# Kernel tuning notes

Hardware: AMD Instinct MI355X
Metric: run time of the kernel (lower is better)

The kernel has to match this reference:

```python
import jax, jax.numpy as jnp
import numpy as np

BATCH, SEQ, DIM = 4, 4096, 256
DT_RANK, D_STATE, NUM_TOKENS = 16, 16, 1024


def _adapool(x, T):
    # uniform window mean == AdaptiveAvgPool1d when S % T == 0
    B, S, D = x.shape
    return x.reshape(B, T, S // T, D).mean(axis=2)


def _layernorm(x, g, b, eps=1e-5):
    mu = x.mean(-1, keepdims=True)
    var = ((x - mu) ** 2).mean(-1, keepdims=True)
    return (x - mu) * jax.lax.rsqrt(var + eps) * g + b


def _gauss_mask(T):
    c = (T + 1) // 2
    idx = jnp.arange(T, dtype=jnp.float32)
    sigma = jnp.abs(idx - c).mean()
    w = jnp.exp(-0.5 * (idx - c) ** 2 / sigma ** 2)
    return w / w.sum()


def _ssm(x, Wdbc, Wdt, bdt, Alog, D):
    A = -jnp.exp(Alog)                                     # (Dm, N)
    dbc = x @ Wdbc.T                                       # (B,L,dt+2N)
    delta = jax.nn.softplus(dbc[..., :DT_RANK] @ Wdt.T + bdt)   # (B,L,Dm)
    Bm = dbc[..., DT_RANK:DT_RANK + D_STATE]               # (B,L,N)
    Cm = dbc[..., DT_RANK + D_STATE:]                      # (B,L,N)
    deltaA = jnp.exp(delta[..., None] * A)                 # (B,L,Dm,N)
    BX = (delta[..., None] * Bm[:, :, None, :]) * x[..., None]
    def comb(c1, c2):
        a1, x1 = c1
        a2, x2 = c2
        return (a2 * a1, a2 * x1 + x2)
    _, hs = jax.lax.associative_scan(comb, (deltaA, BX), axis=1)
    y = jnp.einsum('bldn,bln->bld', hs, Cm) + D * x
    return y


def setup_inputs():
    key = jax.random.key(0)
    ks = jax.random.split(key, 16)
    s = 0.05
    Alog = jnp.tile(jnp.log(jnp.arange(1.0, D_STATE + 1.0, dtype=jnp.float32))[None, :], (DIM, 1))
    return {
        'x': jax.random.normal(ks[0], (BATCH, SEQ, DIM), jnp.float32),
        'ln_g': jnp.ones((DIM,), jnp.float32),
        'ln_b': jnp.zeros((DIM,), jnp.float32),
        'W1': jax.random.normal(ks[1], (DIM, DIM), jnp.float32) * s,
        'b1': jnp.zeros((DIM,), jnp.float32),
        'W2': jax.random.normal(ks[2], (DIM, DIM), jnp.float32) * s,
        'b2': jnp.zeros((DIM,), jnp.float32),
        'Wcf': jax.random.normal(ks[3], (DIM, DIM), jnp.float32) * s,
        'bcf': jnp.zeros((DIM,), jnp.float32),
        'Wcb': jax.random.normal(ks[4], (DIM, DIM), jnp.float32) * s,
        'bcb': jnp.zeros((DIM,), jnp.float32),
        'Wdbc_f': jax.random.normal(ks[5], (DT_RANK + 2 * D_STATE, DIM), jnp.float32) * s,
        'Wdt_f': jax.random.normal(ks[6], (DIM, DT_RANK), jnp.float32) * s,
        'bdt_f': jnp.zeros((DIM,), jnp.float32),
        'Alog_f': Alog,
        'D_f': jnp.ones((DIM,), jnp.float32),
        'Wdbc_b': jax.random.normal(ks[7], (DT_RANK + 2 * D_STATE, DIM), jnp.float32) * s,
        'Wdt_b': jax.random.normal(ks[8], (DIM, DT_RANK), jnp.float32) * s,
        'bdt_b': jnp.zeros((DIM,), jnp.float32),
        'Alog_b': Alog,
        'D_b': jnp.ones((DIM,), jnp.float32),
    }


def reference(x, ln_g, ln_b, W1, b1, W2, b2, Wcf, bcf, Wcb, bcb,
              Wdbc_f, Wdt_f, bdt_f, Alog_f, D_f,
              Wdbc_b, Wdt_b, bdt_b, Alog_b, D_b):
    skip = _adapool(x, NUM_TOKENS)
    xn = _layernorm(x, ln_g, ln_b)
    z = xn @ W1.T + b1
    xp = xn @ W2.T + b2
    mask = _gauss_mask(NUM_TOKENS)[None, :, None]

    # forward direction: 1x1 conv (= channel linear) -> softplus -> SSM
    h1 = jax.nn.softplus(jnp.einsum('bsd,ed->bse', xp, Wcf) + bcf)
    x1 = _ssm(h1, Wdbc_f, Wdt_f, bdt_f, Alog_f, D_f)
    x1 = jax.nn.silu(_adapool(x1, NUM_TOKENS) * mask)

    # backward direction on flipped sequence
    h2 = jax.nn.softplus(jnp.einsum('bsd,ed->bse', xp[:, ::-1], Wcb) + bcb)
    x2 = _ssm(h2, Wdbc_b, Wdt_b, bdt_b, Alog_b, D_b)[:, ::-1]
    x2 = jax.nn.silu(_adapool(x2, NUM_TOKENS) * mask)

    zp = jax.nn.silu(_adapool(z, NUM_TOKENS))
    return zp * x1 + zp * x2 + skip
```

## Files before the change

### kernel.cpp

```cpp
#include <hip/hip_runtime.h>
#include <math.h>


namespace {
constexpr int BB = 4;
constexpr int LL = 4096;
constexpr int DD = 256;
constexpr int NS = 16;
constexpr int NCH = 128;
constexpr int CLEN = 32;
constexpr int NG  = CLEN / 8;
constexpr int TOK = 1024;

constexpr size_t NROW = (size_t)BB * LL;
constexpr size_t NE   = NROW * DD;
constexpr size_t NP   = (size_t)BB * TOK * DD;
constexpr size_t NBC  = NROW * NS;
constexpr size_t NAGG = 2ull * BB * DD * NCH * NS;
constexpr size_t NSD  = 2ull * BB * NCH * DD;

constexpr size_t O_H1X  = 0;
constexpr size_t O_G2X  = NE / 2;
constexpr size_t O_H1T  = NE;
constexpr size_t O_G2T  = NE + NE / 2;
constexpr size_t O_DLTF = 2 * NE;
constexpr size_t O_XN   = O_DLTF;
constexpr size_t O_DLTB = 2 * NE + NE / 2;
constexpr size_t O_BMF  = 3 * NE;
constexpr size_t O_CMF  = O_BMF + NBC;
constexpr size_t O_BMB  = O_CMF + NBC;
constexpr size_t O_CMB  = O_BMB + NBC;
constexpr size_t O_ZP   = O_CMB + NBC;
constexpr size_t O_WF1  = O_ZP + NP;
constexpr size_t O_BF1  = O_WF1 + 768 * 256 / 2;
constexpr size_t O_WF2F = O_BF1 + 768;
constexpr size_t O_B2F  = O_WF2F + 384 * 256 / 2;
constexpr size_t O_WF2B = O_B2F + 384;
constexpr size_t O_B2B  = O_WF2B + 384 * 256 / 2;
constexpr size_t O_SD   = O_B2B + 384;
constexpr size_t O_HEND = O_SD + NSD;
constexpr size_t O_HIN  = O_HEND + NAGG / 2;
constexpr size_t O_MASK = O_HIN + NAGG / 2;

constexpr int SST = 136;
constexpr int NWPREP = 1282;
}

typedef __bf16 bf16x8 __attribute__((ext_vector_type(8)));
typedef __bf16 bf16x4 __attribute__((ext_vector_type(4)));
typedef float f32x4 __attribute__((ext_vector_type(4)));

__device__ __forceinline__ float softplusf(float x) {
    return fmaxf(x, 0.f) + __logf(1.f + __expf(-fabsf(x)));
}
__device__ __forceinline__ float siluf(float x) {
    return x / (1.f + __expf(-x));
}
__device__ __forceinline__ void gl_lds16(const void* g, void* l) {
    __builtin_amdgcn_global_load_lds((const __attribute__((address_space(1))) unsigned int*)g,
                                     (__attribute__((address_space(3))) unsigned int*)l, 16, 0, 0);
}
__device__ __forceinline__ int st_addr(int col, int row) {
    return col * SST + ((((row >> 3) ^ (col >> 3)) & 15) << 3) + (row & 7);
}
__device__ __forceinline__ void pow_chain(float e1, float* p) {
    p[0] = e1;
    p[1] = e1 * e1;
    p[2] = p[1] * e1;
    p[3] = p[1] * p[1];
    p[4] = p[3] * p[0];
    p[5] = p[3] * p[1];
    p[6] = p[3] * p[2];
    p[7] = p[3] * p[3];
    p[8]  = p[7] * p[0];
    p[9]  = p[7] * p[1];
    p[10] = p[7] * p[2];
    p[11] = p[7] * p[3];
    p[12] = p[7] * p[4];
    p[13] = p[7] * p[5];
    p[14] = p[7] * p[6];
    p[15] = p[7] * p[7];
}

#define GEMM_KLOOP(SHBASE, GA, GB, WR, WC, WV, LANE, ACC)                          \
    {                                                                               \
        _Pragma("unroll")                                                           \
        for (int rg = 0; rg < 2; ++rg) {                                            \
            gl_lds16((GA) + rg * 16 * 256, &(SHBASE)[((WV) * 2 + rg) * 512]);       \
            gl_lds16((GB) + rg * 16 * 256, &(SHBASE)[4096 + ((WV) * 2 + rg) * 512]);\
        }                                                                           \
        _Pragma("unroll")                                                           \
        for (int kst = 0; kst < 8; ++kst) {                                         \
            if (kst < 7) {                                                          \
                __bf16* Asn = (SHBASE) + ((kst + 1) & 1) * 8192;                    \
                int k0n = (kst + 1) * 32;                                           \
                _Pragma("unroll")                                                   \
                for (int rg = 0; rg < 2; ++rg) {                                    \
                    gl_lds16((GA) + rg * 16 * 256 + k0n, &Asn[((WV) * 2 + rg) * 512]);      \
                    gl_lds16((GB) + rg * 16 * 256 + k0n, &Asn[4096 + ((WV) * 2 + rg) * 512]);\
                }                                                                   \
                asm volatile("s_waitcnt vmcnt(4)" ::: "memory");                    \
            } else {                                                                \
                asm volatile("s_waitcnt vmcnt(0)" ::: "memory");                    \
            }                                                                       \
            __builtin_amdgcn_s_barrier();                                           \
            __builtin_amdgcn_sched_barrier(0);                                      \
            const __bf16* Ac = (SHBASE) + (kst & 1) * 8192;                         \
            const __bf16* Bc = Ac + 4096;                                           \
            bf16x8 af[4], bfr[4];                                                   \
            _Pragma("unroll")                                                       \
            for (int i = 0; i < 4; ++i)                                             \
                af[i] = *(const bf16x8*)&Ac[((WR) * 4 + i) * 512 + (LANE) * 8];     \
            _Pragma("unroll")                                                       \
            for (int j = 0; j < 4; ++j)                                             \
                bfr[j] = *(const bf16x8*)&Bc[((WC) * 4 + j) * 512 + (LANE) * 8];    \
            __builtin_amdgcn_s_setprio(1);                                          \
            _Pragma("unroll")                                                       \
            for (int i = 0; i < 4; ++i)                                             \
                _Pragma("unroll")                                                   \
                for (int j = 0; j < 4; ++j)                                         \
                    ACC[i][j] = __builtin_amdgcn_mfma_f32_16x16x32_bf16(af[i], bfr[j], ACC[i][j], 0, 0, 0); \
            __builtin_amdgcn_s_setprio(0);                                          \
            __builtin_amdgcn_s_barrier();                                           \
        }                                                                           \
    }

__global__ __launch_bounds__(256) void prep_ln_kernel(
    const float* __restrict__ x, const float* __restrict__ lng, const float* __restrict__ lnb,
    const float* __restrict__ W1, const float* __restrict__ b1,
    const float* __restrict__ W2, const float* __restrict__ b2,
    const float* __restrict__ Wcf, const float* __restrict__ bcf,
    const float* __restrict__ Wcb, const float* __restrict__ bcb,
    const float* __restrict__ Wdt_f, const float* __restrict__ Wdbc_f, const float* __restrict__ bdt_f,
    const float* __restrict__ Wdt_b, const float* __restrict__ Wdbc_b, const float* __restrict__ bdt_b,
    __bf16* __restrict__ xn, float* __restrict__ outp,
    __bf16* __restrict__ Wf1, float* __restrict__ bf1,
    __bf16* __restrict__ Wf2f, float* __restrict__ b2f,
    __bf16* __restrict__ Wf2b, float* __restrict__ b2b,
    float* __restrict__ mask)
{
    int bxg = blockIdx.x;
    int k = threadIdx.x;
    if (bxg >= NWPREP) {
        __shared__ float ls[4][256];
        int r0 = (bxg - NWPREP) * 4;
        int w = k >> 6, l = k & 63;
        int row = r0 + w;
        float4 v = *(const float4*)&x[(size_t)row * 256 + l * 4];
        float s = v.x + v.y + v.z + v.w;
        float q = v.x * v.x + v.y * v.y + v.z * v.z + v.w * v.w;
        for (int o = 32; o > 0; o >>= 1) {
            s += __shfl_xor(s, o, 64);
            q += __shfl_xor(q, o, 64);
        }
        float mu = s * (1.f / 256.f);
        float rs = rsqrtf(q * (1.f / 256.f) - mu * mu + 1e-5f);
        float4 g4 = *(const float4*)&lng[l * 4];
        float4 b4 = *(const float4*)&lnb[l * 4];
        bf16x4 o4;
        o4[0] = (__bf16)((v.x - mu) * rs * g4.x + b4.x);
        o4[1] = (__bf16)((v.y - mu) * rs * g4.y + b4.y);
        o4[2] = (__bf16)((v.z - mu) * rs * g4.z + b4.z);
        o4[3] = (__bf16)((v.w - mu) * rs * g4.w + b4.w);
        *(bf16x4*)&xn[(size_t)row * 256 + l * 4] = o4;
        *(float4*)&ls[w][l * 4] = v;
        __syncthreads();
        int b = r0 >> 12;
        int g = (r0 & 4095) >> 2;
        float acc = ls[0][k] + ls[1][k] + ls[2][k] + ls[3][k];
        outp[((size_t)b * TOK + g) * 256 + k] = acc * 0.25f;
        return;
    }
    int j2 = bxg;
    int mat = j2 / 641;
    int bx = j2 % 641;
    if (bx < 256) {
        int j = bx;
        const float* Wc = mat ? Wcb : Wcf;
        float acc = 0.f, accb = 0.f;
#pragma unroll 8
        for (int m = 0; m < 256; ++m) {
            float w = Wc[j * 256 + m];
            acc  = fmaf(w, W2[m * 256 + k], acc);
            accb = fmaf(w, b2[m], accb);
        }
        Wf1[(size_t)(256 + mat * 256 + j) * 256 + k] = (__bf16)acc;
        if (k == 0) bf1[256 + mat * 256 + j] = accb + (mat ? bcb[j] : bcf[j]);
        if (mat == 0) {
            Wf1[(size_t)j * 256 + k] = (__bf16)W1[j * 256 + k];
            if (k == 0) bf1[j] = b1[j];
        }
    } else if (bx < 640) {
        int j = bx - 256;
        const float* Wdt  = mat ? Wdt_b : Wdt_f;
        const float* Wdbc = mat ? Wdbc_b : Wdbc_f;
        const float* bdt  = mat ? bdt_b : bdt_f;
        __bf16* Wf2 = mat ? Wf2b : Wf2f;
        float* b2x  = mat ? b2b : b2f;
        float val;
        if (j < 256) {
            float acc = 0.f;
#pragma unroll
            for (int m = 0; m < 16; ++m)
                acc = fmaf(Wdt[j * 16 + m], Wdbc[m * 256 + k], acc);
            val = acc;
        } else if (j < 288) {
            val = Wdbc[(16 + (j - 256)) * 256 + k];
        } else {
            val = 0.f;
        }
        Wf2[(size_t)j * 256 + k] = (__bf16)val;
        if (k == 0) b2x[j] = (j < 256) ? bdt[j] : 0.f;
    } else if (mat == 0) {
        __shared__ float red2[4];
        __shared__ float sb;
        float w[4];
        float loc = 0.f;
#pragma unroll
        for (int q = 0; q < 4; ++q) {
            float dd = (float)(k + 256 * q) - 512.f;
            w[q] = __expf(-0.5f * dd * dd * (1.f / 65536.f));
            loc += w[q];
        }
        for (int o = 32; o > 0; o >>= 1) loc += __shfl_xor(loc, o, 64);
        if ((k & 63) == 0) red2[k >> 6] = loc;
        __syncthreads();
        if (k == 0) sb = red2[0] + red2[1] + red2[2] + red2[3];
        __syncthreads();
        float inv = 1.f / sb;
#pragma unroll
        for (int q = 0; q < 4; ++q) mask[k + 256 * q] = w[q] * inv;
    }
}

__global__ __launch_bounds__(256) void gemm1_mfma(
    const __bf16* __restrict__ A, const __bf16* __restrict__ Bw, const float* __restrict__ bias,
    float* __restrict__ zp, __bf16* __restrict__ h1x, __bf16* __restrict__ g2x,
    __bf16* __restrict__ h1T, __bf16* __restrict__ g2T)
{
    __shared__ __align__(16) __bf16 SH[128 * SST];
    int tid = threadIdx.x;
    int lane = tid & 63, wv = tid >> 6;
    int wr = wv >> 1, wc = wv & 1;
    int lm = lane & 15, lq = lane >> 4;
    int m0 = blockIdx.x << 7, n0 = blockIdx.y << 7;

    const __bf16* gaB = A  + (size_t)(m0 + wv * 32 + lm) * 256 + lq * 8;
    const __bf16* gbB = Bw + (size_t)(n0 + wv * 32 + lm) * 256 + lq * 8;

    f32x4 acc[4][4];
#pragma unroll
    for (int i = 0; i < 4; ++i)
#pragma unroll
        for (int j = 0; j < 4; ++j) acc[i][j] = 0;

    GEMM_KLOOP(SH, gaB, gbB, wr, wc, wv, lane, acc)

    int target = blockIdx.y >> 1;
    int colbase = (blockIdx.y & 1) * 128;
    __syncthreads();
    if (target == 0) {
        float* zs = (float*)SH;
#pragma unroll
        for (int j = 0; j < 4; ++j) {
            int coll = wc * 64 + j * 16 + lm;
            float bv = bias[n0 + coll];
#pragma unroll
            for (int i = 0; i < 4; ++i) {
                int gl = wr * 16 + i * 4 + lq;
                float s = acc[i][j][0] + acc[i][j][1] + acc[i][j][2] + acc[i][j][3];
                zs[gl * 132 + coll] = siluf(0.25f * s + bv);
            }
        }
        __syncthreads();
        int b = m0 >> 12, g0 = (m0 & 4095) >> 2;
        int rl = tid >> 5;
        int c4 = (tid & 31) * 4;
#pragma unroll
        for (int p = 0; p < 4; ++p) {
            int g = p * 8 + rl;
            float4 v = *(float4*)&zs[g * 132 + c4];
            *(float4*)&zp[((size_t)b * TOK + g0 + g) * 256 + colbase + c4] = v;
        }
    } else {
        __bf16* hs = SH;
#pragma unroll
        for (int j = 0; j < 4; ++j) {
            int coll = wc * 64 + j * 16 + lm;
            float bv = bias[n0 + coll];
#pragma unroll
            for (int i = 0; i < 4; ++i) {
                int rl = wr * 64 + i * 16 + lq * 4;
                bf16x4 v4;
#pragma unroll
                for (int r = 0; r < 4; ++r)
                    v4[r] = (__bf16)softplusf(acc[i][j][r] + bv);
                *(bf16x4*)&hs[st_addr(coll, rl)] = v4;
            }
        }
        __syncthreads();
        __bf16* outp = (target == 1) ? h1x : g2x;
        __bf16* outT = (target == 1) ? h1T : g2T;
        {
            int tg = tid >> 4;
#pragma unroll
            for (int it = 0; it < 8; ++it) {
                int dcol = it * 16 + (tid & 15);
                bf16x8 v = *(const bf16x8*)&hs[dcol * SST + (((tg ^ (dcol >> 3)) & 15) << 3)];
                *(bf16x8*)&outT[(((size_t)(m0 >> 3) + tg) * 256 + colbase + dcol) * 8] = v;
            }
        }
        {
            int rl2 = tid >> 4;
            int c8 = (tid & 15) * 8;
#pragma unroll
            for (int p = 0; p < 8; ++p) {
                int row = p * 16 + rl2;
                bf16x8 v;
#pragma unroll
                for (int e = 0; e < 8; ++e) v[e] = hs[st_addr(c8 + e, row)];
                *(bf16x8*)&outp[(size_t)(m0 + row) * 256 + colbase + c8] = v;
            }
        }
    }
}

__global__ __launch_bounds__(256) void gemm2_mfma(
    const __bf16* __restrict__ h1x, const __bf16* __restrict__ g2x,
    const __bf16* __restrict__ Wf, const float* __restrict__ bf2,
    const __bf16* __restrict__ Wb, const float* __restrict__ bb2,
    __bf16* __restrict__ dTf, __bf16* __restrict__ dTb,
    float* __restrict__ BmF, float* __restrict__ CmF,
    float* __restrict__ BmB, float* __restrict__ CmB)
{
    __shared__ __align__(16) __bf16 SH[128 * SST];
    int tid = threadIdx.x;
    int lane = tid & 63, wv = tid >> 6;
    int wr = wv >> 1, wc = wv & 1;
    int lm = lane & 15, lq = lane >> 4;
    int m0 = blockIdx.x << 7, n0 = blockIdx.y << 7;
    int dir = blockIdx.z;
    const __bf16* A    = dir ? g2x : h1x;
    const __bf16* Bw   = dir ? Wb : Wf;
    const float* bias  = dir ? bb2 : bf2;
    __bf16* dT = dir ? dTb : dTf;
    float* Bm = dir ? BmB : BmF;
    float* Cm = dir ? CmB : CmF;

    const __bf16* gaB = A  + (size_t)(m0 + wv * 32 + lm) * 256 + lq * 8;
    const __bf16* gbB = Bw + (size_t)(n0 + wv * 32 + lm) * 256 + lq * 8;

    f32x4 acc[4][4];
#pragma unroll
    for (int i = 0; i < 4; ++i)
#pragma unroll
        for (int j = 0; j < 4; ++j) acc[i][j] = 0;

    GEMM_KLOOP(SH, gaB, gbB, wr, wc, wv, lane, acc)

    __syncthreads();
    if (blockIdx.y < 2) {
        __bf16* hs = SH;
        int colbase = blockIdx.y * 128;
#pragma unroll
        for (int j = 0; j < 4; ++j) {
            int coll = wc * 64 + j * 16 + lm;
            float bv = bias[n0 + coll];
#pragma unroll
            for (int i = 0; i < 4; ++i) {
                int rl = wr * 64 + i * 16 + lq * 4;
                bf16x4 v4;
#pragma unroll
                for (int r = 0; r < 4; ++r)
                    v4[r] = (__bf16)softplusf(acc[i][j][r] + bv);
                *(bf16x4*)&hs[st_addr(coll, rl)] = v4;
            }
        }
        __syncthreads();
        int tg = tid >> 4;
#pragma unroll
        for (int it = 0; it < 8; ++it) {
            int dcol = it * 16 + (tid & 15);
            bf16x8 v = *(const bf16x8*)&hs[dcol * SST + (((tg ^ (dcol >> 3)) & 15) << 3)];
            *(bf16x8*)&dT[(((size_t)(m0 >> 3) + tg) * 256 + colbase + dcol) * 8] = v;
        }
    } else {
        float* bs_ = (float*)SH;
        float* cs_ = (float*)SH + 128 * 24;
        if (wc == 0) {
#pragma unroll
            for (int j = 0; j < 2; ++j) {
                int coll = j * 16 + lm;
                float bv = bias[n0 + coll];
                float* dst = j ? cs_ : bs_;
#pragma unroll
                for (int i = 0; i < 4; ++i) {
                    int rl = wr * 64 + i * 16 + lq * 4;
#pragma unroll
                    for (int r = 0; r < 4; ++r)
                        dst[(rl + r) * 24 + lm] = acc[i][j][r] + bv;
                }
            }
        }
        __syncthreads();
        int row = tid >> 1;
        int h8 = (tid & 1) * 8;
        float4 vb0 = *(float4*)&bs_[row * 24 + h8];
        float4 vb1 = *(float4*)&bs_[row * 24 + h8 + 4];
        float4 vc0 = *(float4*)&cs_[row * 24 + h8];
        float4 vc1 = *(float4*)&cs_[row * 24 + h8 + 4];
        *(float4*)&Bm[(size_t)(m0 + row) * 16 + h8]     = vb0;
        *(float4*)&Bm[(size_t)(m0 + row) * 16 + h8 + 4] = vb1;
        *(float4*)&Cm[(size_t)(m0 + row) * 16 + h8]     = vc0;
        *(float4*)&Cm[(size_t)(m0 + row) * 16 + h8 + 4] = vc1;
    }
}

__global__ __launch_bounds__(256) void scan1_kernel(
    const __bf16* __restrict__ dTf, const __bf16* __restrict__ dTb,
    const __bf16* __restrict__ xTf, const __bf16* __restrict__ xTb,
    const float* __restrict__ bmf, const float* __restrict__ bmb,
    const float* __restrict__ alogf, const float* __restrict__ alogb,
    float* __restrict__ sdb, __bf16* __restrict__ hend)
{
    int d = threadIdx.x;
    int c = blockIdx.x, b = blockIdx.y, dir = blockIdx.z;
    const __bf16* dT = dir ? dTb : dTf;
    const __bf16* xT = dir ? xTb : xTf;
    const float* Bm = dir ? bmb : bmf;
    const float* Alog = dir ? alogb : alogf;

    float A[16];
    bool intOK = true;
#pragma unroll
    for (int n = 0; n < 16; ++n) {
        A[n] = -__expf(Alog[(size_t)d * 16 + n]);
        intOK = intOK && (fabsf(A[n] + (float)(n + 1)) < 1e-3f);
    }
    float h[16];
#pragma unroll
    for (int n = 0; n < 16; ++n) h[n] = 0.f;
    float sd = 0.f;
    size_t rg0 = (size_t)b * 512 + (size_t)c * NG;
    size_t rowb = (size_t)b * LL + (size_t)c * CLEN;
    if (intOK) {
        for (int g = 0; g < NG; ++g) {
            int gg = dir ? (NG - 1 - g) : g;
            size_t ti = ((rg0 + gg) * 256 + d) * 8;
            bf16x8 dv = *(const bf16x8*)&dT[ti];
            bf16x8 xv8 = *(const bf16x8*)&xT[ti];
#pragma unroll
            for (int ii = 0; ii < 8; ++ii) {
                int i = dir ? (7 - ii) : ii;
                float dlt = (float)dv[i];
                float xv  = (float)xv8[i];
                float common = dlt * xv;
                sd += dlt;
                float p[16];
                pow_chain(__expf(-dlt), p);
                const f32x4* Bp = (const f32x4*)&Bm[(rowb + gg * 8 + i) * NS];
                f32x4 B0 = Bp[0], B1 = Bp[1], B2 = Bp[2], B3 = Bp[3];
#pragma unroll
                for (int n = 0; n < 4; ++n) {
                    h[n]      = fmaf(p[n],      h[n],      common * B0[n]);
                    h[n + 4]  = fmaf(p[n + 4],  h[n + 4],  common * B1[n]);
                    h[n + 8]  = fmaf(p[n + 8],  h[n + 8],  common * B2[n]);
                    h[n + 12] = fmaf(p[n + 12], h[n + 12], common * B3[n]);
                }
            }
        }
    } else {
        for (int g = 0; g < NG; ++g) {
            int gg = dir ? (NG - 1 - g) : g;
            size_t ti = ((rg0 + gg) * 256 + d) * 8;
            bf16x8 dv = *(const bf16x8*)&dT[ti];
            bf16x8 xv8 = *(const bf16x8*)&xT[ti];
#pragma unroll
            for (int ii = 0; ii < 8; ++ii) {
                int i = dir ? (7 - ii) : ii;
                float dlt = (float)dv[i];
                float xv  = (float)xv8[i];
                float common = dlt * xv;
                sd += dlt;
                const f32x4* Bp = (const f32x4*)&Bm[(rowb + gg * 8 + i) * NS];
                f32x4 B0 = Bp[0], B1 = Bp[1], B2 = Bp[2], B3 = Bp[3];
#pragma unroll
                for (int n = 0; n < 4; ++n) {
                    h[n]      = fmaf(__expf(dlt * A[n]),      h[n],      common * B0[n]);
                    h[n + 4]  = fmaf(__expf(dlt * A[n + 4]),  h[n + 4],  common * B1[n]);
                    h[n + 8]  = fmaf(__expf(dlt * A[n + 8]),  h[n + 8],  common * B2[n]);
                    h[n + 12] = fmaf(__expf(dlt * A[n + 12]), h[n + 12], common * B3[n]);
                }
            }
        }
    }
    size_t sbase = (size_t)(dir * 4 + b) * NCH + c;
    sdb[sbase * 256 + d] = sd;
    size_t hb = sbase * 16 * 256 + d;
#pragma unroll
    for (int n = 0; n < 16; ++n) hend[hb + (size_t)n * 256] = (__bf16)h[n];
}

__global__ __launch_bounds__(128) void scan2_kernel(
    const float* __restrict__ sdb, const __bf16* __restrict__ hend,
    const float* __restrict__ alogf, const float* __restrict__ alogb,
    __bf16* __restrict__ hin)
{
    int blk = blockIdx.x >> 1;
    int n = blk & 15, b = (blk >> 4) & 3, dir = blk >> 6;
    int d = ((blockIdx.x & 1) << 7) + threadIdx.x;
    const float* Alog = dir ? alogb : alogf;
    float A_dn = -__expf(Alog[(size_t)d * 16 + n]);
    size_t basec = (size_t)(dir * 4 + b) * NCH;
    float s = 0.f;
    if (!dir) {
#pragma unroll 8
        for (int c = 0; c < NCH; ++c) {
            float sdv = sdb[(basec + c) * 256 + d];
            size_t idx = ((basec + c) * 16 + n) * 256 + d;
            float he = (float)hend[idx];
            hin[idx] = (__bf16)s;
            s = fmaf(__expf(sdv * A_dn), s, he);
        }
    } else {
#pragma unroll 8
        for (int c = NCH - 1; c >= 0; --c) {
            float sdv = sdb[(basec + c) * 256 + d];
            size_t idx = ((basec + c) * 16 + n) * 256 + d;
            float he = (float)hend[idx];
            hin[idx] = (__bf16)s;
            s = fmaf(__expf(sdv * A_dn), s, he);
        }
    }
}

__global__ __launch_bounds__(256) void scan3_kernel(
    const __bf16* __restrict__ dTf, const __bf16* __restrict__ dTb,
    const __bf16* __restrict__ xTf, const __bf16* __restrict__ xTb,
    const float* __restrict__ bmf, const float* __restrict__ bmb,
    const float* __restrict__ cmf, const float* __restrict__ cmb,
    const float* __restrict__ alogf, const float* __restrict__ alogb,
    const float* __restrict__ Dfp, const float* __restrict__ Dbp,
    const __bf16* __restrict__ hin,
    const float* __restrict__ zp, const float* __restrict__ mask,
    float* __restrict__ outp)
{
    int d = threadIdx.x;
    int c = blockIdx.x, b = blockIdx.y, dir = blockIdx.z;
    const __bf16* dT = dir ? dTb : dTf;
    const __bf16* xT = dir ? xTb : xTf;
    const float* Bm = dir ? bmb : bmf;
    const float* Cm = dir ? cmb : cmf;
    const float* Alog = dir ? alogb : alogf;
    const float* Dv   = dir ? Dbp : Dfp;

    float A[16];
    bool intOK = true;
#pragma unroll
    for (int n = 0; n < 16; ++n) {
        A[n] = -__expf(Alog[(size_t)d * 16 + n]);
        intOK = intOK && (fabsf(A[n] + (float)(n + 1)) < 1e-3f);
    }
    float Dd = Dv[d];
    float h[16];
    size_t hb = ((size_t)(dir * 4 + b) * NCH + c) * 16 * 256 + d;
#pragma unroll
    for (int n = 0; n < 16; ++n) h[n] = (float)hin[hb + (size_t)n * 256];

    size_t rg0 = (size_t)b * 512 + (size_t)c * NG;
    size_t rowb = (size_t)b * LL + (size_t)c * CLEN;
    int base = c * CLEN;
    float pool = 0.f;
    if (intOK) {
        for (int g = 0; g < NG; ++g) {
            int gg = dir ? (NG - 1 - g) : g;
            size_t ti = ((rg0 + gg) * 256 + d) * 8;
            bf16x8 dv = *(const bf16x8*)&dT[ti];
            bf16x8 xv8 = *(const bf16x8*)&xT[ti];
#pragma unroll
            for (int ii = 0; ii < 8; ++ii) {
                int i = dir ? (7 - ii) : ii;
                float dlt = (float)dv[i];
                float xv  = (float)xv8[i];
                float common = dlt * xv;
                float p[16];
                pow_chain(__expf(-dlt), p);
                size_t row = rowb + gg * 8 + i;
                const f32x4* Bp = (const f32x4*)&Bm[row * NS];
                const f32x4* Cp = (const f32x4*)&Cm[row * NS];
                f32x4 B0 = Bp[0], B1 = Bp[1], B2 = Bp[2], B3 = Bp[3];
                f32x4 C0 = Cp[0], C1 = Cp[1], C2 = Cp[2], C3 = Cp[3];
                float y0 = 0.f, y1 = 0.f, y2 = 0.f, y3 = 0.f;
#pragma unroll
                for (int n = 0; n < 4; ++n) {
                    h[n]      = fmaf(p[n],      h[n],      common * B0[n]);
                    h[n + 4]  = fmaf(p[n + 4],  h[n + 4],  common * B1[n]);
                    h[n + 8]  = fmaf(p[n + 8],  h[n + 8],  common * B2[n]);
                    h[n + 12] = fmaf(p[n + 12], h[n + 12], common * B3[n]);
                    y0 = fmaf(h[n],      C0[n], y0);
                    y1 = fmaf(h[n + 4],  C1[n], y1);
                    y2 = fmaf(h[n + 8],  C2[n], y2);
                    y3 = fmaf(h[n + 12], C3[n], y3);
                }
                pool += (y0 + y1) + (y2 + y3) + Dd * xv;
                int t = base + gg * 8 + i;
                bool gend = dir ? ((t & 3) == 0) : ((t & 3) == 3);
                if (gend) {
                    int gtok = t >> 2;
                    size_t ip = ((size_t)b * TOK + gtok) * 256 + d;
                    float contrib = zp[ip] * siluf(pool * 0.25f * mask[gtok]);
                    atomicAdd(&outp[ip], contrib);
                    pool = 0.f;
                }
            }
        }
    } else {
        for (int g = 0; g < NG; ++g) {
            int gg = dir ? (NG - 1 - g) : g;
            size_t ti = ((rg0 + gg) * 256 + d) * 8;
            bf16x8 dv = *(const bf16x8*)&dT[ti];
            bf16x8 xv8 = *(const bf16x8*)&xT[ti];
#pragma unroll
            for (int ii = 0; ii < 8; ++ii) {
                int i = dir ? (7 - ii) : ii;
                float dlt = (float)dv[i];
                float xv  = (float)xv8[i];
                float common = dlt * xv;
                size_t row = rowb + gg * 8 + i;
                const f32x4* Bp = (const f32x4*)&Bm[row * NS];
                const f32x4* Cp = (const f32x4*)&Cm[row * NS];
                f32x4 B0 = Bp[0], B1 = Bp[1], B2 = Bp[2], B3 = Bp[3];
                f32x4 C0 = Cp[0], C1 = Cp[1], C2 = Cp[2], C3 = Cp[3];
                float y0 = 0.f, y1 = 0.f, y2 = 0.f, y3 = 0.f;
#pragma unroll
                for (int n = 0; n < 4; ++n) {
                    h[n]      = fmaf(__expf(dlt * A[n]),      h[n],      common * B0[n]);
                    h[n + 4]  = fmaf(__expf(dlt * A[n + 4]),  h[n + 4],  common * B1[n]);
                    h[n + 8]  = fmaf(__expf(dlt * A[n + 8]),  h[n + 8],  common * B2[n]);
                    h[n + 12] = fmaf(__expf(dlt * A[n + 12]), h[n + 12], common * B3[n]);
                    y0 = fmaf(h[n],      C0[n], y0);
                    y1 = fmaf(h[n + 4],  C1[n], y1);
                    y2 = fmaf(h[n + 8],  C2[n], y2);
                    y3 = fmaf(h[n + 12], C3[n], y3);
                }
                pool += (y0 + y1) + (y2 + y3) + Dd * xv;
                int t = base + gg * 8 + i;
                bool gend = dir ? ((t & 3) == 0) : ((t & 3) == 3);
                if (gend) {
                    int gtok = t >> 2;
                    size_t ip = ((size_t)b * TOK + gtok) * 256 + d;
                    float contrib = zp[ip] * siluf(pool * 0.25f * mask[gtok]);
                    atomicAdd(&outp[ip], contrib);
                    pool = 0.f;
                }
            }
        }
    }
}

extern "C" void kernel_launch(void* const* d_in, const int* in_sizes, int n_in,
                              void* d_out, int out_size, void* d_ws, size_t ws_size,
                              hipStream_t stream)
{
    const float* x      = (const float*)d_in[0];
    const float* ln_g   = (const float*)d_in[1];
    const float* ln_b   = (const float*)d_in[2];
    const float* W1     = (const float*)d_in[3];
    const float* b1     = (const float*)d_in[4];
    const float* W2     = (const float*)d_in[5];
    const float* b2     = (const float*)d_in[6];
    const float* Wcf    = (const float*)d_in[7];
    const float* bcf    = (const float*)d_in[8];
    const float* Wcb    = (const float*)d_in[9];
    const float* bcb    = (const float*)d_in[10];
    const float* Wdbc_f = (const float*)d_in[11];
    const float* Wdt_f  = (const float*)d_in[12];
    const float* bdt_f  = (const float*)d_in[13];
    const float* Alog_f = (const float*)d_in[14];
    const float* D_f    = (const float*)d_in[15];
    const float* Wdbc_b = (const float*)d_in[16];
    const float* Wdt_b  = (const float*)d_in[17];
    const float* bdt_b  = (const float*)d_in[18];
    const float* Alog_b = (const float*)d_in[19];
    const float* D_b    = (const float*)d_in[20];
    float* out = (float*)d_out;
    float* ws  = (float*)d_ws;

    __bf16* h1x = (__bf16*)(ws + O_H1X);
    __bf16* g2x = (__bf16*)(ws + O_G2X);
    __bf16* h1T = (__bf16*)(ws + O_H1T);
    __bf16* g2T = (__bf16*)(ws + O_G2T);
    __bf16* xnb = (__bf16*)(ws + O_XN);
    __bf16* dTf = (__bf16*)(ws + O_DLTF);
    __bf16* dTb = (__bf16*)(ws + O_DLTB);
    float* bmf = ws + O_BMF;
    float* cmf = ws + O_CMF;
    float* bmb = ws + O_BMB;
    float* cmb = ws + O_CMB;
    float* zpb  = ws + O_ZP;
    __bf16* wf1 = (__bf16*)(ws + O_WF1);
    float* bf1  = ws + O_BF1;
    __bf16* wf2f = (__bf16*)(ws + O_WF2F);
    float* b2f  = ws + O_B2F;
    __bf16* wf2b = (__bf16*)(ws + O_WF2B);
    float* b2b  = ws + O_B2B;
    float* sdb  = ws + O_SD;
    __bf16* hnd = (__bf16*)(ws + O_HEND);
    __bf16* hin = (__bf16*)(ws + O_HIN);
    float* mkb  = ws + O_MASK;

    prep_ln_kernel<<<dim3(4096 + NWPREP), 256, 0, stream>>>(
        x, ln_g, ln_b,
        W1, b1, W2, b2, Wcf, bcf, Wcb, bcb,
        Wdt_f, Wdbc_f, bdt_f, Wdt_b, Wdbc_b, bdt_b,
        xnb, out, wf1, bf1, wf2f, b2f, wf2b, b2b, mkb);
    gemm1_mfma<<<dim3(128, 6), 256, 0, stream>>>(xnb, wf1, bf1, zpb, h1x, g2x, h1T, g2T);
    gemm2_mfma<<<dim3(128, 3, 2), 256, 0, stream>>>(h1x, g2x, wf2f, b2f, wf2b, b2b,
                                                    dTf, dTb, bmf, cmf, bmb, cmb);
    scan1_kernel<<<dim3(NCH, BB, 2), 256, 0, stream>>>(dTf, dTb, h1T, g2T, bmf, bmb,
                                                       Alog_f, Alog_b, sdb, hnd);
    scan2_kernel<<<256, 128, 0, stream>>>(sdb, hnd, Alog_f, Alog_b, hin);
    scan3_kernel<<<dim3(NCH, BB, 2), 256, 0, stream>>>(dTf, dTb, h1T, g2T, bmf, bmb, cmf, cmb,
                                                       Alog_f, Alog_b, D_f, D_b, hin,
                                                       zpb, mkb, out);
}
```

Baseline: 207.2 us.

## Split scan3 state dimension across two thread halves with LDS reduction

The scan3 kernel now runs 512 threads per block, and each half handles 8 of the 16 SSM state channels for the same d. This halves per-thread register state and serial FMA/exp work, giving more parallelism across the 1024-block grid. The upper half's pooled partial sums are combined through shared memory with a __syncthreads at each pooling boundary. The cost is extra barriers, duplicated loads of delta and x per thread pair, and an extra multiply by s[7] for the upper half.

```diff
diff --git a/kernel.cpp b/kernel.cpp
--- a/kernel.cpp
+++ b/kernel.cpp
@@ -80,6 +80,16 @@
     p[13] = p[7] * p[5];
     p[14] = p[7] * p[6];
     p[15] = p[7] * p[7];
+}
+__device__ __forceinline__ void pow_chain8(float e1, float* s) {
+    s[0] = e1;
+    s[1] = e1 * e1;
+    s[2] = s[1] * e1;
+    s[3] = s[1] * s[1];
+    s[4] = s[3] * s[0];
+    s[5] = s[3] * s[1];
+    s[6] = s[3] * s[2];
+    s[7] = s[3] * s[3];
 }
 
 #define GEMM_KLOOP(SHBASE, GA, GB, WR, WC, WV, LANE, ACC)                          \
@@ -534,7 +544,7 @@
     }
 }
 
-__global__ __launch_bounds__(256) void scan3_kernel(
+__global__ __launch_bounds__(512) void scan3_kernel(
     const __bf16* __restrict__ dTf, const __bf16* __restrict__ dTb,
     const __bf16* __restrict__ xTf, const __bf16* __restrict__ xTb,
     const float* __restrict__ bmf, const float* __restrict__ bmb,
@@ -545,7 +555,10 @@
     const float* __restrict__ zp, const float* __restrict__ mask,
     float* __restrict__ outp)
 {
-    int d = threadIdx.x;
+    __shared__ float ls1[8 * 256];
+    int tid = threadIdx.x;
+    int d = tid & 255;
+    int half = tid >> 8;
     int c = blockIdx.x, b = blockIdx.y, dir = blockIdx.z;
     const __bf16* dT = dir ? dTb : dTf;
     const __bf16* xT = dir ? xTb : xTf;
@@ -554,18 +567,19 @@
     const float* Alog = dir ? alogb : alogf;
     const float* Dv   = dir ? Dbp : Dfp;
 
-    float A[16];
+    float A_h[8];
     bool intOK = true;
 #pragma unroll
     for (int n = 0; n < 16; ++n) {
-        A[n] = -__expf(Alog[(size_t)d * 16 + n]);
-        intOK = intOK && (fabsf(A[n] + (float)(n + 1)) < 1e-3f);
-    }
-    float Dd = Dv[d];
-    float h[16];
+        float a = -__expf(Alog[(size_t)d * 16 + n]);
+        intOK = intOK && (fabsf(a + (float)(n + 1)) < 1e-3f);
+        if ((n >> 3) == half) A_h[n & 7] = a;
+    }
+    float Dd = half ? 0.f : Dv[d];
+    float h[8];
     size_t hb = ((size_t)(dir * 4 + b) * NCH + c) * 16 * 256 + d;
 #pragma unroll
-    for (int n = 0; n < 16; ++n) h[n] = (float)hin[hb + (size_t)n * 256];
+    for (int j = 0; j < 8; ++j) h[j] = (float)hin[hb + (size_t)(half * 8 + j) * 256];
 
     size_t rg0 = (size_t)b * 512 + (size_t)c * NG;
     size_t rowb = (size_t)b * LL + (size_t)c * CLEN;
@@ -583,33 +597,36 @@
                 float dlt = (float)dv[i];
                 float xv  = (float)xv8[i];
                 float common = dlt * xv;
-                float p[16];
-                pow_chain(__expf(-dlt), p);
+                float s[8];
+                pow_chain8(__expf(-dlt), s);
+                float pm = half ? s[7] : 1.f;
                 size_t row = rowb + gg * 8 + i;
-                const f32x4* Bp = (const f32x4*)&Bm[row * NS];
-                const f32x4* Cp = (const f32x4*)&Cm[row * NS];
-                f32x4 B0 = Bp[0], B1 = Bp[1], B2 = Bp[2], B3 = Bp[3];
-                f32x4 C0 = Cp[0], C1 = Cp[1], C2 = Cp[2], C3 = Cp[3];
-                float y0 = 0.f, y1 = 0.f, y2 = 0.f, y3 = 0.f;
+                const f32x4* Bp = (const f32x4*)&Bm[row * NS + half * 8];
+                const f32x4* Cp = (const f32x4*)&Cm[row * NS + half * 8];
+                f32x4 B0 = Bp[0], B1 = Bp[1];
+                f32x4 C0 = Cp[0], C1 = Cp[1];
+                float y0 = 0.f, y1 = 0.f;
 #pragma unroll
                 for (int n = 0; n < 4; ++n) {
-                    h[n]      = fmaf(p[n],      h[n],      common * B0[n]);
-                    h[n + 4]  = fmaf(p[n + 4],  h[n + 4],  common * B1[n]);
-                    h[n + 8]  = fmaf(p[n + 8],  h[n + 8],  common * B2[n]);
-                    h[n + 12] = fmaf(p[n + 12], h[n + 12], common * B3[n]);
-                    y0 = fmaf(h[n],      C0[n], y0);
-                    y1 = fmaf(h[n + 4],  C1[n], y1);
-                    y2 = fmaf(h[n + 8],  C2[n], y2);
-                    y3 = fmaf(h[n + 12], C3[n], y3);
+                    h[n]     = fmaf(s[n] * pm,     h[n],     common * B0[n]);
+                    h[n + 4] = fmaf(s[n + 4] * pm, h[n + 4], common * B1[n]);
+                    y0 = fmaf(h[n],     C0[n], y0);
+                    y1 = fmaf(h[n + 4], C1[n], y1);
                 }
-                pool += (y0 + y1) + (y2 + y3) + Dd * xv;
+                pool += y0 + y1 + Dd * xv;
                 int t = base + gg * 8 + i;
                 bool gend = dir ? ((t & 3) == 0) : ((t & 3) == 3);
                 if (gend) {
                     int gtok = t >> 2;
-                    size_t ip = ((size_t)b * TOK + gtok) * 256 + d;
-                    float contrib = zp[ip] * siluf(pool * 0.25f * mask[gtok]);
-                    atomicAdd(&outp[ip], contrib);
+                    int gl = gtok - (c << 3);
+                    if (half) ls1[(gl << 8) + d] = pool;
+                    __syncthreads();
+                    if (!half) {
+                        float tot = pool + ls1[(gl << 8) + d];
+                        size_t ip = ((size_t)b * TOK + gtok) * 256 + d;
+                        float contrib = zp[ip] * siluf(tot * 0.25f * mask[gtok]);
+                        atomicAdd(&outp[ip], contrib);
+                    }
                     pool = 0.f;
                 }
             }
@@ -627,30 +644,32 @@
                 float xv  = (float)xv8[i];
                 float common = dlt * xv;
                 size_t row = rowb + gg * 8 + i;
-                const f32x4* Bp = (const f32x4*)&Bm[row * NS];
-                const f32x4* Cp = (const f32x4*)&Cm[row * NS];
-                f32x4 B0 = Bp[0], B1 = Bp[1], B2 = Bp[2], B3 = Bp[3];
-                f32x4 C0 = Cp[0], C1 = Cp[1], C2 = Cp[2], C3 = Cp[3];
-                float y0 = 0.f, y1 = 0.f, y2 = 0.f, y3 = 0.f;
+                const f32x4* Bp = (const f32x4*)&Bm[row * NS + half * 8];
+                const f32x4* Cp = (const f32x4*)&Cm[row * NS + half * 8];
+                f32x4 B0 = Bp[0], B1 = Bp[1];
+                f32x4 C0 = Cp[0], C1 = Cp[1];
+                float y0 = 0.f, y1 = 0.f;
 #pragma unroll
                 for (int n = 0; n < 4; ++n) {
-                    h[n]      = fmaf(__expf(dlt * A[n]),      h[n],      common * B0[n]);
-                    h[n + 4]  = fmaf(__expf(dlt * A[n + 4]),  h[n + 4],  common * B1[n]);
-                    h[n + 8]  = fmaf(__expf(dlt * A[n + 8]),  h[n + 8],  common * B2[n]);
-                    h[n + 12] = fmaf(__expf(dlt * A[n + 12]), h[n + 12], common * B3[n]);
-                    y0 = fmaf(h[n],      C0[n], y0);
-                    y1 = fmaf(h[n + 4],  C1[n], y1);
-                    y2 = fmaf(h[n + 8],  C2[n], y2);
-                    y3 = fmaf(h[n + 12], C3[n], y3);
+                    h[n]     = fmaf(__expf(dlt * A_h[n]),     h[n],     common * B0[n]);
+                    h[n + 4] = fmaf(__expf(dlt * A_h[n + 4]), h[n + 4], common * B1[n]);
+                    y0 = fmaf(h[n],     C0[n], y0);
+                    y1 = fmaf(h[n + 4], C1[n], y1);
                 }
-                pool += (y0 + y1) + (y2 + y3) + Dd * xv;
+                pool += y0 + y1 + Dd * xv;
                 int t = base + gg * 8 + i;
                 bool gend = dir ? ((t & 3) == 0) : ((t & 3) == 3);
                 if (gend) {
                     int gtok = t >> 2;
-                    size_t ip = ((size_t)b * TOK + gtok) * 256 + d;
-                    float contrib = zp[ip] * siluf(pool * 0.25f * mask[gtok]);
-                    atomicAdd(&outp[ip], contrib);
+                    int gl = gtok - (c << 3);
+                    if (half) ls1[(gl << 8) + d] = pool;
+                    __syncthreads();
+                    if (!half) {
+                        float tot = pool + ls1[(gl << 8) + d];
+                        size_t ip = ((size_t)b * TOK + gtok) * 256 + d;
+                        float contrib = zp[ip] * siluf(tot * 0.25f * mask[gtok]);
+                        atomicAdd(&outp[ip], contrib);
+                    }
                     pool = 0.f;
                 }
             }
@@ -720,7 +739,7 @@
     scan1_kernel<<<dim3(NCH, BB, 2), 256, 0, stream>>>(dTf, dTb, h1T, g2T, bmf, bmb,
                                                        Alog_f, Alog_b, sdb, hnd);
     scan2_kernel<<<256, 128, 0, stream>>>(sdb, hnd, Alog_f, Alog_b, hin);
-    scan3_kernel<<<dim3(NCH, BB, 2), 256, 0, stream>>>(dTf, dTb, h1T, g2T, bmf, bmb, cmf, cmb,
+    scan3_kernel<<<dim3(NCH, BB, 2), 512, 0, stream>>>(dTf, dTb, h1T, g2T, bmf, bmb, cmf, cmb,
                                                        Alog_f, Alog_b, D_f, D_b, hin,
                                                        zpb, mkb, out);
 }
```

Result: slower. 223.6 us (+7.9%).
